# Performance work log

Measured on AMD Instinct MI355X. Metric: run time of the kernel, lower is better.

Reference implementation:

```python
import jax, jax.numpy as jnp
import numpy as np

M_POW = 4   # m: number of visual-graph powers
N_POW = 4   # n: number of text-graph powers
T = 32      # temporal length, forced by torch.eye(32) in GraphFusion
EPS_BN = 1e-5


def conv1d_same(x, w, b):
    # x: (B, Cin, L), w: (Cout, Cin, 3) -> (B, Cout, L), padding=1
    y = jax.lax.conv_general_dilated(x, w, window_strides=(1,), padding=[(1, 1)],
                                     dimension_numbers=("NCH", "OIH", "NCH"))
    return y + b[None, :, None]


def setup_inputs() -> dict:
    key = jax.random.key(0)
    ks = jax.random.split(key, 10)
    b, c = 128, 5
    d = {}
    d["v_feature"] = jax.random.normal(ks[0], (b, c, T, 2048), jnp.float32)
    d["t_feature"] = jax.random.normal(ks[1], (b, c, T, 768), jnp.float32)
    # Temporal embedding convs (Conv1d k=3, pad=1)
    d["wv"] = jax.random.normal(ks[2], (32, 2048, 3), jnp.float32) * 0.02
    d["bv"] = jnp.zeros((32,), jnp.float32)
    d["wt"] = jax.random.normal(ks[3], (32, 768, 3), jnp.float32) * 0.02
    d["bt"] = jnp.zeros((32,), jnp.float32)
    # GraphFusion learned (m, n) bilinear matrix: torch.normal(0, 1)
    d["fusion_a"] = jax.random.normal(ks[4], (M_POW, N_POW), jnp.float32)
    # NormalHead (BN-WVAD style, in_channel=32, hidden 2 -> 1 -> 1, all k=1 convs)
    d["w1"] = jax.random.normal(ks[5], (2, 32), jnp.float32) * 0.1
    d["b1"] = jnp.zeros((2,), jnp.float32)
    d["g1"] = jnp.ones((2,), jnp.float32)
    d["be1"] = jnp.zeros((2,), jnp.float32)
    d["w2"] = jax.random.normal(ks[6], (1, 2), jnp.float32) * 0.1
    d["b2"] = jnp.zeros((1,), jnp.float32)
    d["g2"] = jnp.ones((1,), jnp.float32)
    d["be2"] = jnp.zeros((1,), jnp.float32)
    d["w3"] = jax.random.normal(ks[7], (1, 1), jnp.float32) * 0.1
    d["b3"] = jnp.zeros((1,), jnp.float32)
    return d


def _forward(v_feature, t_feature, wv, bv, wt, bt, fusion_a,
             w1, b1, g1, be1, w2, b2, g2, be2, w3, b3):
    b, c, t, feat_v = v_feature.shape
    B = b * c
    fv = v_feature.reshape(B, t, feat_v)
    ft = t_feature.reshape(B, t, t_feature.shape[3])
    # Temporal: permute -> conv1d(k=3,pad=1) -> relu -> permute
    fv = jax.nn.relu(conv1d_same(fv.transpose(0, 2, 1), wv, bv)).transpose(0, 2, 1)  # (B,t,32)
    ft = jax.nn.relu(conv1d_same(ft.transpose(0, 2, 1), wt, bt)).transpose(0, 2, 1)  # (B,t,32)

    # GraphFusion
    def l2n(x):
        return x / jnp.maximum(jnp.linalg.norm(x, axis=2, keepdims=True), 1e-12)
    f_v = l2n(fv)
    f_t = l2n(ft)
    a_v = jax.nn.relu(jnp.einsum('bid,bjd->bij', f_v, f_v))  # (B,t,t)
    a_t = jax.nn.relu(jnp.einsum('bid,bjd->bij', f_t, f_t))  # (B,t,t)
    eye = jnp.broadcast_to(jnp.eye(t, dtype=a_v.dtype), (B, t, t))
    # power 0 replaced by identity, as in the torch code
    av_p = jnp.stack([eye] + [a_v ** i for i in range(1, M_POW)], axis=0)  # (m,B,t,t)
    at_p = jnp.stack([eye] + [a_t ** j for j in range(1, N_POW)], axis=0)  # (n,B,t,t)
    # einsum('bijk,kl,blij->bij') with the permutes undone == 'kbij,kl,lbij->bij'
    a_fused = jnp.einsum('kbij,kl,lbij->bij', av_p, fusion_a, at_p)
    a_fused = jax.nn.relu(a_fused)
    a_fused = a_fused / (jnp.max(a_fused) + 0.01)

    # NormalHead on x = a_fused.permute(0,2,1) : (B, C=t, L=t)
    x = a_fused.transpose(0, 2, 1)

    def bn(h, g, beta):  # training-mode BatchNorm1d over (N, L) per channel
        mu = h.mean(axis=(0, 2), keepdims=True)
        var = h.var(axis=(0, 2), keepdims=True)
        return (h - mu) * jax.lax.rsqrt(var + EPS_BN) * g[None, :, None] + beta[None, :, None]

    x1 = jnp.einsum('oc,bcl->bol', w1, x) + b1[None, :, None]
    h1 = jax.nn.relu(bn(x1, g1, be1))
    x2 = jnp.einsum('oc,bcl->bol', w2, h1) + b2[None, :, None]
    h2 = jax.nn.relu(bn(x2, g2, be2))
    scores = jax.nn.sigmoid(jnp.einsum('oc,bcl->bol', w3, h2) + b3[None, :, None])  # (B,1,t)
    normal_scores = scores.reshape(b, c, t).mean(axis=1)  # (b, t), crop-averaged
    return (normal_scores, a_v, a_t, a_fused)


def reference(v_feature, t_feature, wv, bv, wt, bt, fusion_a,
              w1, b1, g1, be1, w2, b2, g2, be2, w3, b3):
    return _forward(v_feature, t_feature, wv, bv, wt, bt, fusion_a,
                    w1, b1, g1, be1, w2, b2, g2, be2, w3, b3)
```

## Files before the change

kernel.cpp:

```cpp
#include <hip/hip_runtime.h>
#include <hip/hip_bf16.h>
#include <math.h>


typedef __attribute__((ext_vector_type(8))) short short8;
typedef __attribute__((ext_vector_type(4))) float f32x4;

#define XROW 132

__device__ __forceinline__ unsigned short f2bf(float f) {
    __hip_bfloat16 h = __float2bfloat16(f);
    return *reinterpret_cast<unsigned short*>(&h);
}
__device__ __forceinline__ float bf2f(unsigned short u) {
    return __uint_as_float(((unsigned int)u) << 16);
}
__device__ __forceinline__ short8 lds_frag(const unsigned short* p) {
    union { uint2 u2[2]; short8 s; } r;
    r.u2[0] = *reinterpret_cast<const uint2*>(p);
    r.u2[1] = *reinterpret_cast<const uint2*>(p + 4);
    return r.s;
}
__device__ __forceinline__ short8 glb_frag(const unsigned short* p) {
    union { uint4 u; short8 s; } r;
    r.u = *reinterpret_cast<const uint4*>(p);
    return r.s;
}

__global__ __launch_bounds__(256) void pack_kernel(
    const float* __restrict__ wv, const float* __restrict__ wt,
    unsigned short* __restrict__ wvpk, unsigned short* __restrict__ wtpk,
    float* __restrict__ scal, float* __restrict__ zbuf, int nz) {
    int gid = blockIdx.x * 256 + threadIdx.x;
    if (gid < 16) scal[gid] = 0.f;
    for (int i = gid; i < nz; i += gridDim.x * 256) zbuf[i] = 0.f;
    const int NV = 196608, NT = 73728;
    if (gid < NV) {
        int o = gid / 6144, rem = gid % 6144;
        int c = rem / 3, k = rem % 3;
        int s = c >> 5, cp = c & 31;
        float f = wv[gid];
        unsigned short h = f2bf(f);
        unsigned short l = f2bf(f - bf2f(h));
        int base = (s * 3 + k) * 2048 + o * 32 + cp;
        wvpk[base] = h;
        wvpk[base + 1024] = l;
    } else if (gid < NV + NT) {
        int g = gid - NV;
        int o = g / 2304, rem = g % 2304;
        int c = rem / 3, k = rem % 3;
        int s = c >> 5, cp = c & 31;
        float f = wt[g];
        unsigned short h = f2bf(f);
        unsigned short l = f2bf(f - bf2f(h));
        int base = (s * 3 + k) * 2048 + o * 32 + cp;
        wtpk[base] = h;
        wtpk[base + 1024] = l;
    }
}

__global__ __launch_bounds__(256, 8) void conv_mfma_kernel(
    const float* __restrict__ xv, const unsigned short* __restrict__ wvpk,
    const float* __restrict__ xt, const unsigned short* __restrict__ wtpk,
    float* __restrict__ yv, float* __restrict__ yt) {
    __shared__ unsigned short hiT[34 * XROW], loT[34 * XROW];
    int bid = blockIdx.x;
    const float* x; const unsigned short* wpk; float* y;
    int Cin, b, c0g, nchunk;
    if (bid < 2560) {
        x = xv; wpk = wvpk; y = yv; Cin = 2048;
        b = bid >> 2; c0g = (bid & 3) << 9; nchunk = 4;
    } else {
        int tb = bid - 2560;
        x = xt; wpk = wtpk; y = yt; Cin = 768;
        b = tb >> 1; c0g = (tb & 1) * 384; nchunk = 3;
    }
    int tid = threadIdx.x, wave = tid >> 6, lane = tid & 63;
    if (tid < XROW) {
        hiT[tid] = 0; hiT[33 * XROW + tid] = 0;
        loT[tid] = 0; loT[33 * XROW + tid] = 0;
    }
    f32x4 acc0 = {0.f, 0.f, 0.f, 0.f};
    f32x4 acc1 = {0.f, 0.f, 0.f, 0.f};
    int tm = wave & 1, tn = wave >> 1;
    int m = lane & 15, quad = lane >> 4;
    int c4 = tid & 31, tg = tid >> 5;
    const float* xb = x + (size_t)b * 32 * Cin + c0g;
    for (int ch = 0; ch < nchunk; ++ch) {
        int c0 = ch << 7;
        if (ch) __syncthreads();
#pragma unroll
        for (int pass = 0; pass < 4; ++pass) {
            int t = tg + (pass << 3);
            const float4 xq = *reinterpret_cast<const float4*>(
                xb + (size_t)t * Cin + c0 + (c4 << 2));
            unsigned short h0 = f2bf(xq.x), h1 = f2bf(xq.y);
            unsigned short h2 = f2bf(xq.z), h3 = f2bf(xq.w);
            unsigned short l0 = f2bf(xq.x - bf2f(h0));
            unsigned short l1 = f2bf(xq.y - bf2f(h1));
            unsigned short l2 = f2bf(xq.z - bf2f(h2));
            unsigned short l3 = f2bf(xq.w - bf2f(h3));
            int widx = (t + 1) * XROW + (c4 << 2);
            *reinterpret_cast<uint2*>(hiT + widx) =
                make_uint2(h0 | ((unsigned int)h1 << 16), h2 | ((unsigned int)h3 << 16));
            *reinterpret_cast<uint2*>(loT + widx) =
                make_uint2(l0 | ((unsigned int)l1 << 16), l2 | ((unsigned int)l3 << 16));
        }
        __syncthreads();
        int sbase = (c0g + c0) >> 5;
        int arow0 = (tm << 4) + m;
        int bofs = ((tn << 4) + m) * 32 + (quad << 3);
#pragma unroll
        for (int sl = 0; sl < 4; ++sl) {
            int acol = (sl << 5) + (quad << 3);
            const unsigned short* bbase = wpk + (size_t)(sbase + sl) * 6144 + bofs;
#pragma unroll
            for (int k = 0; k < 3; ++k) {
                short8 Ah = lds_frag(hiT + (arow0 + k) * XROW + acol);
                short8 Al = lds_frag(loT + (arow0 + k) * XROW + acol);
                short8 Bh = glb_frag(bbase + k * 2048);
                short8 Bl = glb_frag(bbase + k * 2048 + 1024);
                acc0 = __builtin_amdgcn_mfma_f32_16x16x32_bf16(Ah, Bh, acc0, 0, 0, 0);
                acc1 = __builtin_amdgcn_mfma_f32_16x16x32_bf16(Ah, Bl, acc1, 0, 0, 0);
                acc1 = __builtin_amdgcn_mfma_f32_16x16x32_bf16(Al, Bh, acc1, 0, 0, 0);
            }
        }
    }
    int ocol = (tn << 4) + m;
#pragma unroll
    for (int r = 0; r < 4; ++r) {
        int t = (tm << 4) + (quad << 2) + r;
        atomicAdd(&y[(size_t)b * 1024 + t * 32 + ocol], acc0[r] + acc1[r]);
    }
}

__global__ __launch_bounds__(256) void s2_kernel(
    const float* __restrict__ fvp, const float* __restrict__ ftp,
    const float* __restrict__ bv, const float* __restrict__ bt,
    const float* __restrict__ fuse, float* __restrict__ out_av,
    float* __restrict__ out_at, float* __restrict__ out_af,
    unsigned int* __restrict__ maxslot) {
    int b = blockIdx.x, tid = threadIdx.x;
    __shared__ float Fv[32][33], Ft[32][33], inv[64], wmax[4];
#pragma unroll
    for (int e = 0; e < 4; ++e) {
        int idx = tid + 256 * e;
        int i = idx >> 5, j = idx & 31;
        Fv[i][j] = fmaxf(fvp[b * 1024 + idx] + bv[j], 0.f);
        Ft[i][j] = fmaxf(ftp[b * 1024 + idx] + bt[j], 0.f);
    }
    __syncthreads();
    {
        int row = tid >> 3, cg = (tid & 7) * 4;
        float sv = 0.f, st = 0.f;
#pragma unroll
        for (int q = 0; q < 4; ++q) {
            float v = Fv[row][cg + q]; sv = fmaf(v, v, sv);
            float u = Ft[row][cg + q]; st = fmaf(u, u, st);
        }
        sv += __shfl_xor(sv, 1); sv += __shfl_xor(sv, 2); sv += __shfl_xor(sv, 4);
        st += __shfl_xor(st, 1); st += __shfl_xor(st, 2); st += __shfl_xor(st, 4);
        if ((tid & 7) == 0) {
            inv[row]      = rsqrtf(fmaxf(sv, 1e-24f));
            inv[32 + row] = rsqrtf(fmaxf(st, 1e-24f));
        }
    }
    __syncthreads();
    float fa[16];
#pragma unroll
    for (int q = 0; q < 16; ++q) fa[q] = fuse[q];
    float lmax = 0.f;
#pragma unroll
    for (int e = 0; e < 4; ++e) {
        int idx = tid + 256 * e;
        int i = idx >> 5, j = idx & 31;
        float dv = 0.f, dt_ = 0.f;
        for (int c = 0; c < 32; ++c) {
            dv  = fmaf(Fv[i][c], Fv[j][c], dv);
            dt_ = fmaf(Ft[i][c], Ft[j][c], dt_);
        }
        float av = fmaxf(dv  * inv[i] * inv[j], 0.f);
        float at = fmaxf(dt_ * inv[32 + i] * inv[32 + j], 0.f);
        out_av[b * 1024 + idx] = av;
        out_at[b * 1024 + idx] = at;
        float pv0 = (i == j) ? 1.f : 0.f;
        float pv1 = av, pv2 = av * av, pv3 = pv2 * av;
        float pt1 = at, pt2 = at * at, pt3 = pt2 * at;
        float af = 0.f;
        af += (fa[0] * pv0 + fa[4] * pv1 + fa[8]  * pv2 + fa[12] * pv3) * pv0;
        af += (fa[1] * pv0 + fa[5] * pv1 + fa[9]  * pv2 + fa[13] * pv3) * pt1;
        af += (fa[2] * pv0 + fa[6] * pv1 + fa[10] * pv2 + fa[14] * pv3) * pt2;
        af += (fa[3] * pv0 + fa[7] * pv1 + fa[11] * pv2 + fa[15] * pv3) * pt3;
        float r = fmaxf(af, 0.f);
        out_af[b * 1024 + idx] = r;
        lmax = fmaxf(lmax, r);
    }
    for (int off = 1; off < 64; off <<= 1)
        lmax = fmaxf(lmax, __shfl_xor(lmax, off));
    if ((tid & 63) == 0) wmax[tid >> 6] = lmax;
    __syncthreads();
    if (tid == 0) {
        float mx = fmaxf(fmaxf(wmax[0], wmax[1]), fmaxf(wmax[2], wmax[3]));
        atomicMax(maxslot, __float_as_uint(mx));
    }
}

__global__ __launch_bounds__(256) void s3_kernel(
    float* __restrict__ af, const float* __restrict__ w1,
    const float* __restrict__ b1, float* __restrict__ x1,
    float* __restrict__ scal) {
    int b = blockIdx.x, tid = threadIdx.x;
    __shared__ float A[32][33];
    float inv = 1.0f / (__uint_as_float(((const unsigned int*)scal)[0]) + 0.01f);
#pragma unroll
    for (int e = 0; e < 4; ++e) {
        int idx = tid + 256 * e;
        float v = af[b * 1024 + idx] * inv;
        af[b * 1024 + idx] = v;
        A[idx >> 5][idx & 31] = v;
    }
    __syncthreads();
    if (tid < 64) {
        int o = tid >> 5, l = tid & 31;
        float s = b1[o];
        for (int c = 0; c < 32; ++c) s = fmaf(w1[o * 32 + c], A[l][c], s);
        x1[(size_t)(b * 2 + o) * 32 + l] = s;
        float s1 = s, s2 = s * s;
        for (int off = 1; off < 32; off <<= 1) {
            s1 += __shfl_xor(s1, off);
            s2 += __shfl_xor(s2, off);
        }
        if (l == 0) {
            atomicAdd(&scal[1 + o], s1);
            atomicAdd(&scal[3 + o], s2);
        }
    }
}

__global__ __launch_bounds__(256) void s4_kernel(
    const float* __restrict__ x1, const float* __restrict__ g1,
    const float* __restrict__ be1, const float* __restrict__ w2,
    const float* __restrict__ b2, float* __restrict__ x2,
    float* __restrict__ scal) {
    int idx = blockIdx.x * 256 + threadIdx.x;
    const float N = 20480.f;
    float mu0 = scal[1] / N, mu1 = scal[2] / N;
    float va0 = scal[3] / N - mu0 * mu0, va1 = scal[4] / N - mu1 * mu1;
    float rs0 = rsqrtf(va0 + 1e-5f), rs1 = rsqrtf(va1 + 1e-5f);
    int b = idx >> 5, l = idx & 31;
    float h0 = fmaxf((x1[(size_t)(b * 2 + 0) * 32 + l] - mu0) * rs0 * g1[0] + be1[0], 0.f);
    float h1 = fmaxf((x1[(size_t)(b * 2 + 1) * 32 + l] - mu1) * rs1 * g1[1] + be1[1], 0.f);
    float v = w2[0] * h0 + w2[1] * h1 + b2[0];
    x2[idx] = v;
    float s1 = v, s2 = v * v;
    for (int off = 1; off < 64; off <<= 1) {
        s1 += __shfl_xor(s1, off);
        s2 += __shfl_xor(s2, off);
    }
    __shared__ float ps[4][2];
    int lane = threadIdx.x & 63, w = threadIdx.x >> 6;
    if (lane == 0) { ps[w][0] = s1; ps[w][1] = s2; }
    __syncthreads();
    if (threadIdx.x == 0) {
        atomicAdd(&scal[5], ps[0][0] + ps[1][0] + ps[2][0] + ps[3][0]);
        atomicAdd(&scal[6], ps[0][1] + ps[1][1] + ps[2][1] + ps[3][1]);
    }
}

__global__ __launch_bounds__(256) void s5_kernel(
    const float* __restrict__ x2, const float* __restrict__ g2,
    const float* __restrict__ be2, const float* __restrict__ w3,
    const float* __restrict__ b3, float* __restrict__ ns,
    const float* __restrict__ scal) {
    int idx = blockIdx.x * 256 + threadIdx.x;
    const float N = 20480.f;
    float mu = scal[5] / N;
    float var = scal[6] / N - mu * mu;
    float rs = rsqrtf(var + 1e-5f);
    int bb = idx >> 5, t = idx & 31;
    float s = 0.f;
#pragma unroll
    for (int crop = 0; crop < 5; ++crop) {
        int b = bb * 5 + crop;
        float h = fmaxf((x2[b * 32 + t] - mu) * rs * g2[0] + be2[0], 0.f);
        float z = w3[0] * h + b3[0];
        s += 1.f / (1.f + expf(-z));
    }
    ns[idx] = s * 0.2f;
}

extern "C" void kernel_launch(void* const* d_in, const int* in_sizes, int n_in,
                              void* d_out, int out_size, void* d_ws, size_t ws_size,
                              hipStream_t stream) {
    const float* v_feat = (const float*)d_in[0];
    const float* t_feat = (const float*)d_in[1];
    const float* wv  = (const float*)d_in[2];
    const float* bv  = (const float*)d_in[3];
    const float* wt  = (const float*)d_in[4];
    const float* bt  = (const float*)d_in[5];
    const float* fuse= (const float*)d_in[6];
    const float* w1  = (const float*)d_in[7];
    const float* b1  = (const float*)d_in[8];
    const float* g1  = (const float*)d_in[9];
    const float* be1 = (const float*)d_in[10];
    const float* w2  = (const float*)d_in[11];
    const float* b2  = (const float*)d_in[12];
    const float* g2  = (const float*)d_in[13];
    const float* be2 = (const float*)d_in[14];
    const float* w3  = (const float*)d_in[15];
    const float* b3  = (const float*)d_in[16];

    float* ws   = (float*)d_ws;
    float* scal = ws;
    unsigned short* wvpk = (unsigned short*)(ws + 16);
    unsigned short* wtpk = (unsigned short*)(ws + 16 + 196608);
    float* fv   = ws + 16 + 196608 + 73728;
    float* ft   = fv + 655360;
    float* x1   = ft + 655360;
    float* x2   = x1 + 40960;

    float* out_ns = (float*)d_out;
    float* out_av = out_ns + 4096;
    float* out_at = out_av + 655360;
    float* out_af = out_at + 655360;

    pack_kernel<<<1056, 256, 0, stream>>>(wv, wt, wvpk, wtpk, scal, fv, 2 * 655360);
    conv_mfma_kernel<<<3840, 256, 0, stream>>>(v_feat, wvpk, t_feat, wtpk, fv, ft);
    s2_kernel<<<640, 256, 0, stream>>>(fv, ft, bv, bt, fuse, out_av, out_at,
                                       out_af, (unsigned int*)scal);
    s3_kernel<<<640, 256, 0, stream>>>(out_af, w1, b1, x1, scal);
    s4_kernel<<<80, 256, 0, stream>>>(x1, g1, be1, w2, b2, x2, scal);
    s5_kernel<<<16, 256, 0, stream>>>(x2, g2, be2, w3, b3, out_ns, scal);
}
```

Before: 401.6 us.

## Restructure conv MFMA to per-wave 32x32 tiles with register-prefetched input chunks

Each wave now owns a whole 32x32 output tile over its channel slice and uses 32x32x16 bf16 MFMAs instead of four waves sharing a block tile of 16x16x32 MFMAs. Every wave stages its own 32-channel chunk in private LDS, so block-wide __syncthreads are no longer needed. The next chunk's global loads are issued into registers before the current chunk is computed, to hide memory latency. The costs are more registers (occupancy hint lowered to 4), 16 atomics per lane, and intra-wave LDS reuse that depends on wave lockstep without an explicit barrier.

Result: slower. 414.4 us (+3.2%).

```diff
diff --git a/kernel.cpp b/kernel.cpp
--- a/kernel.cpp
+++ b/kernel.cpp
@@ -3,10 +3,11 @@
 #include <math.h>
 
 
-typedef __attribute__((ext_vector_type(8))) short short8;
-typedef __attribute__((ext_vector_type(4))) float f32x4;
-
-#define XROW 132
+typedef __attribute__((ext_vector_type(8)))  short short8;
+typedef __attribute__((ext_vector_type(4)))  float f32x4;
+typedef __attribute__((ext_vector_type(16))) float f32x16;
+
+#define SROW 40
 
 __device__ __forceinline__ unsigned short f2bf(float f) {
     __hip_bfloat16 h = __float2bfloat16(f);
@@ -15,10 +16,9 @@
 __device__ __forceinline__ float bf2f(unsigned short u) {
     return __uint_as_float(((unsigned int)u) << 16);
 }
-__device__ __forceinline__ short8 lds_frag(const unsigned short* p) {
-    union { uint2 u2[2]; short8 s; } r;
-    r.u2[0] = *reinterpret_cast<const uint2*>(p);
-    r.u2[1] = *reinterpret_cast<const uint2*>(p + 4);
+__device__ __forceinline__ short8 lds_frag16(const unsigned short* p) {
+    union { uint4 u; short8 s; } r;
+    r.u = *reinterpret_cast<const uint4*>(p);
     return r.s;
 }
 __device__ __forceinline__ short8 glb_frag(const unsigned short* p) {
@@ -59,78 +59,93 @@
     }
 }
 
-__global__ __launch_bounds__(256, 8) void conv_mfma_kernel(
+__device__ __forceinline__ void ldx4(float4* q, const float* xb, int Cin,
+                                     int cbase, int r0, int c4f) {
+#pragma unroll
+    for (int p = 0; p < 4; ++p)
+        q[p] = *reinterpret_cast<const float4*>(
+            xb + (size_t)(r0 + 8 * p) * Cin + cbase + c4f);
+}
+
+__device__ __forceinline__ void do_chunk(
+    const float4* q, unsigned short* hiT, unsigned short* loT,
+    const unsigned short* __restrict__ wpk, int s3base, int r0, int c4u,
+    int m, int half, f32x16& acc0, f32x16& acc1) {
+#pragma unroll
+    for (int p = 0; p < 4; ++p) {
+        int r = r0 + 8 * p + 1;
+        float4 v = q[p];
+        unsigned short h0 = f2bf(v.x), h1 = f2bf(v.y);
+        unsigned short h2 = f2bf(v.z), h3 = f2bf(v.w);
+        unsigned short l0 = f2bf(v.x - bf2f(h0));
+        unsigned short l1 = f2bf(v.y - bf2f(h1));
+        unsigned short l2 = f2bf(v.z - bf2f(h2));
+        unsigned short l3 = f2bf(v.w - bf2f(h3));
+        *reinterpret_cast<uint2*>(hiT + r * SROW + c4u) =
+            make_uint2(h0 | ((unsigned int)h1 << 16), h2 | ((unsigned int)h3 << 16));
+        *reinterpret_cast<uint2*>(loT + r * SROW + c4u) =
+            make_uint2(l0 | ((unsigned int)l1 << 16), l2 | ((unsigned int)l3 << 16));
+    }
+#pragma unroll
+    for (int kstep = 0; kstep < 2; ++kstep)
+#pragma unroll
+        for (int tap = 0; tap < 3; ++tap) {
+            const unsigned short* bp = wpk + (size_t)(s3base + tap) * 2048 +
+                                       m * 32 + kstep * 16 + half * 8;
+            short8 Bh = glb_frag(bp);
+            short8 Bl = glb_frag(bp + 1024);
+            int ao = (m + tap) * SROW + kstep * 16 + half * 8;
+            short8 Ah = lds_frag16(hiT + ao);
+            short8 Al = lds_frag16(loT + ao);
+            acc0 = __builtin_amdgcn_mfma_f32_32x32x16_bf16(Ah, Bh, acc0, 0, 0, 0);
+            acc1 = __builtin_amdgcn_mfma_f32_32x32x16_bf16(Ah, Bl, acc1, 0, 0, 0);
+            acc1 = __builtin_amdgcn_mfma_f32_32x32x16_bf16(Al, Bh, acc1, 0, 0, 0);
+        }
+}
+
+__global__ __launch_bounds__(256, 4) void conv_mfma_kernel(
     const float* __restrict__ xv, const unsigned short* __restrict__ wvpk,
     const float* __restrict__ xt, const unsigned short* __restrict__ wtpk,
     float* __restrict__ yv, float* __restrict__ yt) {
-    __shared__ unsigned short hiT[34 * XROW], loT[34 * XROW];
-    int bid = blockIdx.x;
+    __shared__ unsigned short stage[4][2][34 * SROW];
+    int wave = threadIdx.x >> 6, lane = threadIdx.x & 63;
+    int wid = blockIdx.x * 4 + wave;
     const float* x; const unsigned short* wpk; float* y;
     int Cin, b, c0g, nchunk;
-    if (bid < 2560) {
+    if (wid < 2560) {
         x = xv; wpk = wvpk; y = yv; Cin = 2048;
-        b = bid >> 2; c0g = (bid & 3) << 9; nchunk = 4;
+        b = wid >> 2; c0g = (wid & 3) << 9; nchunk = 16;
     } else {
-        int tb = bid - 2560;
+        int tw = wid - 2560;
         x = xt; wpk = wtpk; y = yt; Cin = 768;
-        b = tb >> 1; c0g = (tb & 1) * 384; nchunk = 3;
-    }
-    int tid = threadIdx.x, wave = tid >> 6, lane = tid & 63;
-    if (tid < XROW) {
-        hiT[tid] = 0; hiT[33 * XROW + tid] = 0;
-        loT[tid] = 0; loT[33 * XROW + tid] = 0;
-    }
-    f32x4 acc0 = {0.f, 0.f, 0.f, 0.f};
-    f32x4 acc1 = {0.f, 0.f, 0.f, 0.f};
-    int tm = wave & 1, tn = wave >> 1;
-    int m = lane & 15, quad = lane >> 4;
-    int c4 = tid & 31, tg = tid >> 5;
+        b = tw >> 1; c0g = (tw & 1) * 384; nchunk = 12;
+    }
+    unsigned short* hiT = stage[wave][0];
+    unsigned short* loT = stage[wave][1];
+    if (lane < SROW) {
+        hiT[lane] = 0; hiT[33 * SROW + lane] = 0;
+        loT[lane] = 0; loT[33 * SROW + lane] = 0;
+    }
+    f32x16 acc0 = {0,0,0,0,0,0,0,0,0,0,0,0,0,0,0,0};
+    f32x16 acc1 = {0,0,0,0,0,0,0,0,0,0,0,0,0,0,0,0};
+    int m = lane & 31, half = lane >> 5;
+    int r0 = lane >> 3, c4f = (lane & 7) * 4;
+    int c4u = c4f;
     const float* xb = x + (size_t)b * 32 * Cin + c0g;
-    for (int ch = 0; ch < nchunk; ++ch) {
-        int c0 = ch << 7;
-        if (ch) __syncthreads();
-#pragma unroll
-        for (int pass = 0; pass < 4; ++pass) {
-            int t = tg + (pass << 3);
-            const float4 xq = *reinterpret_cast<const float4*>(
-                xb + (size_t)t * Cin + c0 + (c4 << 2));
-            unsigned short h0 = f2bf(xq.x), h1 = f2bf(xq.y);
-            unsigned short h2 = f2bf(xq.z), h3 = f2bf(xq.w);
-            unsigned short l0 = f2bf(xq.x - bf2f(h0));
-            unsigned short l1 = f2bf(xq.y - bf2f(h1));
-            unsigned short l2 = f2bf(xq.z - bf2f(h2));
-            unsigned short l3 = f2bf(xq.w - bf2f(h3));
-            int widx = (t + 1) * XROW + (c4 << 2);
-            *reinterpret_cast<uint2*>(hiT + widx) =
-                make_uint2(h0 | ((unsigned int)h1 << 16), h2 | ((unsigned int)h3 << 16));
-            *reinterpret_cast<uint2*>(loT + widx) =
-                make_uint2(l0 | ((unsigned int)l1 << 16), l2 | ((unsigned int)l3 << 16));
-        }
-        __syncthreads();
-        int sbase = (c0g + c0) >> 5;
-        int arow0 = (tm << 4) + m;
-        int bofs = ((tn << 4) + m) * 32 + (quad << 3);
-#pragma unroll
-        for (int sl = 0; sl < 4; ++sl) {
-            int acol = (sl << 5) + (quad << 3);
-            const unsigned short* bbase = wpk + (size_t)(sbase + sl) * 6144 + bofs;
-#pragma unroll
-            for (int k = 0; k < 3; ++k) {
-                short8 Ah = lds_frag(hiT + (arow0 + k) * XROW + acol);
-                short8 Al = lds_frag(loT + (arow0 + k) * XROW + acol);
-                short8 Bh = glb_frag(bbase + k * 2048);
-                short8 Bl = glb_frag(bbase + k * 2048 + 1024);
-                acc0 = __builtin_amdgcn_mfma_f32_16x16x32_bf16(Ah, Bh, acc0, 0, 0, 0);
-                acc1 = __builtin_amdgcn_mfma_f32_16x16x32_bf16(Ah, Bl, acc1, 0, 0, 0);
-                acc1 = __builtin_amdgcn_mfma_f32_16x16x32_bf16(Al, Bh, acc1, 0, 0, 0);
-            }
-        }
-    }
-    int ocol = (tn << 4) + m;
-#pragma unroll
-    for (int r = 0; r < 4; ++r) {
-        int t = (tm << 4) + (quad << 2) + r;
-        atomicAdd(&y[(size_t)b * 1024 + t * 32 + ocol], acc0[r] + acc1[r]);
+    int s3g = (c0g >> 5) * 3;
+    float4 qa[4], qb[4];
+    ldx4(qa, xb, Cin, 0, r0, c4f);
+    for (int ch = 0; ch < nchunk; ch += 2) {
+        ldx4(qb, xb, Cin, (ch + 1) << 5, r0, c4f);
+        do_chunk(qa, hiT, loT, wpk, s3g + ch * 3, r0, c4u, m, half, acc0, acc1);
+        if (ch + 2 < nchunk)
+            ldx4(qa, xb, Cin, (ch + 2) << 5, r0, c4f);
+        do_chunk(qb, hiT, loT, wpk, s3g + (ch + 1) * 3, r0, c4u, m, half, acc0, acc1);
+    }
+#pragma unroll
+    for (int reg = 0; reg < 16; ++reg) {
+        int row = (reg & 3) + 8 * (reg >> 2) + 4 * half;
+        atomicAdd(&y[(size_t)b * 1024 + row * 32 + m], acc0[reg] + acc1[reg]);
     }
 }
 
@@ -325,7 +340,7 @@
     float* out_af = out_at + 655360;
 
     pack_kernel<<<1056, 256, 0, stream>>>(wv, wt, wvpk, wtpk, scal, fv, 2 * 655360);
-    conv_mfma_kernel<<<3840, 256, 0, stream>>>(v_feat, wvpk, t_feat, wtpk, fv, ft);
+    conv_mfma_kernel<<<960, 256, 0, stream>>>(v_feat, wvpk, t_feat, wtpk, fv, ft);
     s2_kernel<<<640, 256, 0, stream>>>(fv, ft, bv, bt, fuse, out_av, out_at,
                                        out_af, (unsigned int*)scal);
     s3_kernel<<<640, 256, 0, stream>>>(out_af, w1, b1, x1, scal);
```
